# Kernel optimization log

Measured on AMD Instinct MI355X. Metric: run time of the kernel, lower is better.

Reference implementation:

```python
import jax, jax.numpy as jnp
import numpy as np

L = 3          # num_layers
H = 128        # hidden_dim
NH = 4         # num heads
DH = H // NH   # head dim
B = 32         # graphs per batch
N = 1024       # nodes per graph
NTOT = B * N
DEG = 16
E = NTOT * DEG
BN_EPS = 1e-5


def setup_inputs() -> dict:
    key = jax.random.key(0)
    ks = jax.random.split(key, 16)
    s = 1.0 / np.sqrt(H)
    inp = {
        "x": jax.random.normal(ks[0], (NTOT, H), jnp.float32),
        "edge_attr": jax.random.normal(ks[1], (E, H), jnp.float32),
        "gine_w1": jax.random.normal(ks[2], (L, H, H), jnp.float32) * s,
        "gine_b1": jnp.zeros((L, H), jnp.float32),
        "gine_bn_g": jnp.ones((L, H), jnp.float32),
        "gine_bn_b": jnp.zeros((L, H), jnp.float32),
        "gine_w2": jax.random.normal(ks[3], (L, H, H), jnp.float32) * s,
        "gine_b2": jnp.zeros((L, H), jnp.float32),
        "attn_wqkv": jax.random.normal(ks[4], (L, 3 * H, H), jnp.float32) * s,
        "attn_bqkv": jnp.zeros((L, 3 * H), jnp.float32),
        "attn_wo": jax.random.normal(ks[5], (L, H, H), jnp.float32) * s,
        "attn_bo": jnp.zeros((L, H), jnp.float32),
        "norm1_g": jnp.ones((L, H), jnp.float32),
        "norm1_b": jnp.zeros((L, H), jnp.float32),
        "norm2_g": jnp.ones((L, H), jnp.float32),
        "norm2_b": jnp.zeros((L, H), jnp.float32),
        "norm3_g": jnp.ones((L, H), jnp.float32),
        "norm3_b": jnp.zeros((L, H), jnp.float32),
        "mlp_w1": jax.random.normal(ks[6], (L, 2 * H, H), jnp.float32) * s,
        "mlp_b1": jnp.zeros((L, 2 * H), jnp.float32),
        "mlp_w2": jax.random.normal(ks[7], (L, H, 2 * H), jnp.float32) * (1.0 / np.sqrt(2 * H)),
        "mlp_b2": jnp.zeros((L, H), jnp.float32),
    }
    # intra-graph random edges: local src/dst in [0, N) plus per-graph offset
    offs = (jnp.arange(E, dtype=jnp.int32) // (N * DEG)) * N  # graph offset per edge
    src = jax.random.randint(ks[8], (E,), 0, N, jnp.int32) + offs
    dst = jax.random.randint(ks[9], (E,), 0, N, jnp.int32) + offs
    inp["edge_index"] = jnp.stack([src, dst]).astype(jnp.int32)
    inp["batch"] = (jnp.arange(NTOT, dtype=jnp.int32) // N)
    return inp


def _bn(x, g, b):
    m = x.mean(axis=0)
    v = jnp.var(x, axis=0)
    return (x - m) * jax.lax.rsqrt(v + BN_EPS) * g + b


def _gps_forward(x, edge_attr, gine_w1, gine_b1, gine_bn_g, gine_bn_b, gine_w2, gine_b2,
                 attn_wqkv, attn_bqkv, attn_wo, attn_bo,
                 norm1_g, norm1_b, norm2_g, norm2_b, norm3_g, norm3_b,
                 mlp_w1, mlp_b1, mlp_w2, mlp_b2, edge_index, batch):
    src, dst = edge_index[0], edge_index[1]
    for i in range(L):
        # ---- GINEConv: msg = relu(x_j + e), sum-scatter, nn-MLP on x + aggr (eps=0)
        msg = jax.nn.relu(x[src] + edge_attr)                       # [E, H]
        aggr = jax.ops.segment_sum(msg, dst, num_segments=NTOT)     # [NTOT, H]
        h = x + aggr
        h = h @ gine_w1[i].T + gine_b1[i]
        h = jax.nn.relu(_bn(h, gine_bn_g[i], gine_bn_b[i]))
        h = h @ gine_w2[i].T + gine_b2[i]
        h_local = _bn(h + x, norm1_g[i], norm1_b[i])                # residual + norm1
        # ---- global multi-head attention on x (dense per-graph, equal sizes)
        xb = x.reshape(B, N, H)
        qkv = xb @ attn_wqkv[i].T + attn_bqkv[i]                    # [B, N, 3H]
        q, k, v = jnp.split(qkv, 3, axis=-1)
        q = q.reshape(B, N, NH, DH).transpose(0, 2, 1, 3)           # [B, nh, N, dh]
        k = k.reshape(B, N, NH, DH).transpose(0, 2, 1, 3)
        v = v.reshape(B, N, NH, DH).transpose(0, 2, 1, 3)
        scores = jnp.einsum("bhqd,bhkd->bhqk", q, k) / np.sqrt(DH)
        attn = jax.nn.softmax(scores, axis=-1)
        o = jnp.einsum("bhqk,bhkd->bhqd", attn, v)
        o = o.transpose(0, 2, 1, 3).reshape(B, N, H) @ attn_wo[i].T + attn_bo[i]
        h_attn = _bn(o.reshape(NTOT, H) + x, norm2_g[i], norm2_b[i])
        # ---- combine + FFN + norm3
        out = h_local + h_attn
        ff = jax.nn.relu(out @ mlp_w1[i].T + mlp_b1[i]) @ mlp_w2[i].T + mlp_b2[i]
        x = _bn(out + ff, norm3_g[i], norm3_b[i])
        if i != L - 1:
            x = jax.nn.relu(x)
    return x


def reference(x, edge_attr, gine_w1, gine_b1, gine_bn_g, gine_bn_b, gine_w2, gine_b2,
              attn_wqkv, attn_bqkv, attn_wo, attn_bo,
              norm1_g, norm1_b, norm2_g, norm2_b, norm3_g, norm3_b,
              mlp_w1, mlp_b1, mlp_w2, mlp_b2, edge_index, batch):
    return _gps_forward(x, edge_attr, gine_w1, gine_b1, gine_bn_g, gine_bn_b, gine_w2, gine_b2,
                        attn_wqkv, attn_bqkv, attn_wo, attn_bo,
                        norm1_g, norm1_b, norm2_g, norm2_b, norm3_g, norm3_b,
                        mlp_w1, mlp_b1, mlp_w2, mlp_b2, edge_index, batch)
```

## Files before the change

kernel.cpp:

```cpp
#include <hip/hip_runtime.h>
#include <hip/hip_bf16.h>
#include <math.h>

#define NTOT 32768
#define HDIM 128
#define NE   524288
#define NGRAPH 32
#define NNODE 1024
#define NHEAD 4
#define DHEAD 32

typedef __attribute__((ext_vector_type(8))) short bf8v;
typedef __attribute__((ext_vector_type(4))) float f4v;
typedef unsigned short u16;

__device__ __forceinline__ float4 ld4(const float* p){ return *(const float4*)p; }

__device__ __forceinline__ u16 bf16rn(float f){
  union { float f; unsigned u; } x; x.f = f;
  unsigned r = x.u + 0x7FFF + ((x.u >> 16) & 1);
  return (u16)(r >> 16);
}
__device__ __forceinline__ unsigned pk2(float a, float b){
  unsigned r;
  asm("v_cvt_pk_bf16_f32 %0, %1, %2" : "=v"(r) : "v"(a), "v"(b));
  return r;
}
__device__ __forceinline__ float bf2f(u16 u){
  union { unsigned u; float f; } x; x.u = ((unsigned)u) << 16;
  return x.f;
}

__global__ void k_count(const int* __restrict__ dst, int* __restrict__ deg){
  int e = blockIdx.x*256 + threadIdx.x;
  atomicAdd(&deg[dst[e]], 1);
}

__global__ __launch_bounds__(1024) void k_scan(const int* __restrict__ deg,
                                               int* __restrict__ indptr,
                                               int* __restrict__ cursor){
  __shared__ int sm[1024];
  int t = threadIdx.x;
  int base = t*32;
  int s = 0;
  for (int j=0;j<32;j++) s += deg[base+j];
  sm[t] = s; __syncthreads();
  for (int off=1; off<1024; off<<=1){
    int v = (t>=off) ? sm[t-off] : 0;
    __syncthreads();
    sm[t] += v;
    __syncthreads();
  }
  int ex = sm[t] - s;
  for (int j=0;j<32;j++){
    int d = deg[base+j];
    indptr[base+j] = ex; cursor[base+j] = ex;
    ex += d;
  }
  if (t == 1023) indptr[NTOT] = ex;
}

__global__ void k_fill(const int* __restrict__ dst, int* __restrict__ cursor,
                       int* __restrict__ perm){
  int e = blockIdx.x*256 + threadIdx.x;
  int pos = atomicAdd(&cursor[dst[e]], 1);
  perm[pos] = e;
}

__global__ __launch_bounds__(256) void k_eaprep(const float* __restrict__ ea,
    const int* __restrict__ src, const int* __restrict__ perm,
    u16* __restrict__ EAb, int* __restrict__ SRCp){
  int tid = threadIdx.x;
  int p = blockIdx.x*8 + (tid>>5);
  int c4 = (tid&31)*4;
  int e = perm[p];
  float4 v = ld4(&ea[(size_t)e*HDIM + c4]);
  uint2 o; o.x = pk2(v.x, v.y); o.y = pk2(v.z, v.w);
  *(uint2*)&EAb[(size_t)p*HDIM + c4] = o;
  if ((tid&31) == 0) SRCp[p] = src[e];
}

__global__ __launch_bounds__(256) void k_xprep(const float* __restrict__ x, u16* __restrict__ Xb){
  size_t i = ((size_t)blockIdx.x*256 + threadIdx.x)*4;
  float4 v = ld4(&x[i]);
  uint2 o; o.x = pk2(v.x,v.y); o.y = pk2(v.z,v.w);
  *(uint2*)&Xb[i] = o;
}

__global__ __launch_bounds__(256) void k_wprep(const float* s0,const float* s1,const float* s2,
    const float* s3,const float* s4,const float* s5, u16* __restrict__ Wb){
  const float* srcs[6] = {s0,s1,s2,s3,s4,s5};
  const int cnt4[6] = {12288,12288,36864,12288,24576,24576};
  const int off[6]  = {0,49152,98304,245760,294912,393216};
  int y = blockIdx.y;
  int i = blockIdx.x*256 + threadIdx.x;
  if (i >= cnt4[y]) return;
  float4 v = ld4(&srcs[y][(size_t)i*4]);
  uint2 o; o.x = pk2(v.x,v.y); o.y = pk2(v.z,v.w);
  *(uint2*)&Wb[off[y] + (size_t)i*4] = o;
}

__global__ __launch_bounds__(256) void k_aggr(const u16* __restrict__ Xb,
                       const u16* __restrict__ EAb,
                       const int* __restrict__ SRCp, const int* __restrict__ indptr,
                       u16* __restrict__ Hb){
  int tid = threadIdx.x;
  int n = blockIdx.x*8 + (tid>>5);
  int c4 = (tid&31)*4;
  int p0 = indptr[n], p1 = indptr[n+1];
  float a0=0.f,a1=0.f,a2=0.f,a3=0.f;
  for (int p=p0;p<p1;p++){
    int s = SRCp[p];
    uint2 xv = *(const uint2*)&Xb[(size_t)s*HDIM + c4];
    uint2 ev = *(const uint2*)&EAb[(size_t)p*HDIM + c4];
    a0 += fmaxf(bf2f((u16)(xv.x&0xffff)) + bf2f((u16)(ev.x&0xffff)), 0.f);
    a1 += fmaxf(bf2f((u16)(xv.x>>16))    + bf2f((u16)(ev.x>>16)), 0.f);
    a2 += fmaxf(bf2f((u16)(xv.y&0xffff)) + bf2f((u16)(ev.y&0xffff)), 0.f);
    a3 += fmaxf(bf2f((u16)(xv.y>>16))    + bf2f((u16)(ev.y>>16)), 0.f);
  }
  uint2 xn = *(const uint2*)&Xb[(size_t)n*HDIM + c4];
  a0 += bf2f((u16)(xn.x&0xffff)); a1 += bf2f((u16)(xn.x>>16));
  a2 += bf2f((u16)(xn.y&0xffff)); a3 += bf2f((u16)(xn.y>>16));
  uint2 o; o.x = pk2(a0,a1); o.y = pk2(a2,a3);
  *(uint2*)&Hb[(size_t)n*HDIM + c4] = o;
}

template<bool BNA, bool DUAL, bool RELU, bool EP, bool STATS, bool WROUT>
__global__ __launch_bounds__(256) void k_bgemm(const u16* __restrict__ Ab,
    const u16* __restrict__ A2b,
    const float* __restrict__ slotA, const float* __restrict__ gA, const float* __restrict__ bA,
    const float* __restrict__ slotB, const float* __restrict__ gB, const float* __restrict__ bB,
    const u16* __restrict__ Wb, const float* __restrict__ bias,
    const u16* __restrict__ Epb, u16* __restrict__ Cb,
    u16* __restrict__ OUTb, float* __restrict__ slotOut, int N, int K){
  __shared__ float sbnA[256];
  __shared__ float sbnB[256];
  __shared__ float sred[128];
  int tid = threadIdx.x;
  int w = tid>>6, l = tid&63;
  int q = l&15, g = l>>4;
  int m0 = blockIdx.x*128, n0 = blockIdx.y*64;
  int wr = w*32;
  const float invn = 1.0f/32768.0f;
  if (BNA || DUAL){
    if (tid < 128){
      float mean = slotA[tid]*invn;
      float var  = slotA[128+tid]*invn - mean*mean;
      float sc = gA[tid] * rsqrtf(var + 1e-5f);
      sbnA[tid] = sc; sbnA[128+tid] = bA[tid] - mean*sc;
      if (DUAL){
        float mean2 = slotB[tid]*invn;
        float var2  = slotB[128+tid]*invn - mean2*mean2;
        float sc2 = gB[tid] * rsqrtf(var2 + 1e-5f);
        sbnB[tid] = sc2; sbnB[128+tid] = bB[tid] - mean2*sc2;
      }
    }
  }
  if (STATS && tid < 128) sred[tid] = 0.f;
  if (BNA || DUAL || STATS) __syncthreads();

  f4v acc[2][4];
  #pragma unroll
  for (int i=0;i<2;i++)
    #pragma unroll
    for (int j=0;j<4;j++) acc[i][j] = (f4v){0.f,0.f,0.f,0.f};

  for (int kc=0; kc<K; kc+=32){
    bf8v af[2], bfv[4];
    #pragma unroll
    for (int mt=0;mt<2;mt++){
      int row = m0 + wr + 16*mt + q;
      if (!BNA && !DUAL){
        af[mt] = *(const bf8v*)&Ab[(size_t)row*K + kc + 8*g];
      } else {
        union { bf8v b; u16 s[8]; unsigned u[4]; } ra, r2, ro;
        ra.b = *(const bf8v*)&Ab[(size_t)row*K + kc + 8*g];
        if (DUAL) r2.b = *(const bf8v*)&A2b[(size_t)row*K + kc + 8*g];
        float v[8];
        #pragma unroll
        for (int j=0;j<8;j++){
          int kk = kc + 8*g + j;
          float f = bf2f(ra.s[j]) * sbnA[kk] + sbnA[128+kk];
          if (BNA) f = fmaxf(f, 0.f);
          if (DUAL) f += bf2f(r2.s[j]) * sbnB[kk] + sbnB[128+kk];
          v[j] = f;
        }
        ro.u[0]=pk2(v[0],v[1]); ro.u[1]=pk2(v[2],v[3]);
        ro.u[2]=pk2(v[4],v[5]); ro.u[3]=pk2(v[6],v[7]);
        af[mt] = ro.b;
        if (WROUT && blockIdx.y == 0)
          *(uint4*)&OUTb[(size_t)row*K + kc + 8*g] = *(uint4*)ro.u;
      }
    }
    #pragma unroll
    for (int nt=0;nt<4;nt++){
      int col = n0 + 16*nt + q;
      bfv[nt] = *(const bf8v*)&Wb[(size_t)col*K + kc + 8*g];
    }
    #pragma unroll
    for (int mt=0;mt<2;mt++)
      #pragma unroll
      for (int nt=0;nt<4;nt++)
        acc[mt][nt] = __builtin_amdgcn_mfma_f32_16x16x32_bf16(af[mt], bfv[nt], acc[mt][nt], 0,0,0);
  }
  float bbv[4];
  #pragma unroll
  for (int nt=0;nt<4;nt++) bbv[nt] = bias[n0 + 16*nt + q];
  float csum[4] = {0.f,0.f,0.f,0.f}, csq[4] = {0.f,0.f,0.f,0.f};
  #pragma unroll
  for (int mt=0;mt<2;mt++){
    int row0 = m0 + wr + 16*mt + 4*g;
    #pragma unroll
    for (int nt=0;nt<4;nt++){
      int col = n0 + 16*nt + q;
      #pragma unroll
      for (int r=0;r<4;r++){
        size_t off = (size_t)(row0+r)*N + col;
        float v = acc[mt][nt][r] + bbv[nt];
        if (EP) v += bf2f(Epb[off]);
        if (RELU) v = fmaxf(v, 0.f);
        Cb[off] = bf16rn(v);
        if (STATS){ csum[nt] += v; csq[nt] += v*v; }
      }
    }
  }
  if (STATS){
    #pragma unroll
    for (int nt=0;nt<4;nt++){
      int c = 16*nt + q;
      atomicAdd(&sred[c], csum[nt]);
      atomicAdd(&sred[64+c], csq[nt]);
    }
    __syncthreads();
    if (tid < 64){
      atomicAdd(&slotOut[n0+tid], sred[tid]);
      atomicAdd(&slotOut[128+n0+tid], sred[64+tid]);
    }
  }
}

__global__ __launch_bounds__(256) void k_qkvgemm(const u16* __restrict__ Ab,
    const u16* __restrict__ Wb, const float* __restrict__ bias,
    u16* __restrict__ Qb, u16* __restrict__ Kb, u16* __restrict__ VT){
  __shared__ u16 Sm[128*72];
  int tid = threadIdx.x;
  int w = tid>>6, l = tid&63;
  int q = l&15, g = l>>4;
  int m0 = blockIdx.x*128, n0 = blockIdx.y*64;
  int which = blockIdx.y >> 1, half = blockIdx.y & 1;
  int wr = w*32;
  const int K = 128;
  f4v acc[2][4];
  #pragma unroll
  for (int i=0;i<2;i++)
    #pragma unroll
    for (int j=0;j<4;j++) acc[i][j] = (f4v){0.f,0.f,0.f,0.f};
  for (int kc=0; kc<K; kc+=32){
    bf8v af[2], bfv[4];
    #pragma unroll
    for (int mt=0;mt<2;mt++)
      af[mt] = *(const bf8v*)&Ab[(size_t)(m0+wr+16*mt+q)*K + kc + 8*g];
    #pragma unroll
    for (int nt=0;nt<4;nt++)
      bfv[nt] = *(const bf8v*)&Wb[(size_t)(n0+16*nt+q)*K + kc + 8*g];
    #pragma unroll
    for (int mt=0;mt<2;mt++)
      #pragma unroll
      for (int nt=0;nt<4;nt++)
        acc[mt][nt] = __builtin_amdgcn_mfma_f32_16x16x32_bf16(af[mt], bfv[nt], acc[mt][nt], 0,0,0);
  }
  const float QSC = 0.17677669529663687f * 1.4426950408889634f;
  float scale = (which==0) ? QSC : 1.0f;
  float bbv[4];
  #pragma unroll
  for (int nt=0;nt<4;nt++) bbv[nt] = bias[n0 + 16*nt + q];
  if (which < 2){
    #pragma unroll
    for (int mt=0;mt<2;mt++){
      int row0 = wr + 16*mt + 4*g;
      #pragma unroll
      for (int nt=0;nt<4;nt++){
        int c = 16*nt + q;
        #pragma unroll
        for (int r=0;r<4;r++)
          Sm[(row0+r)*72 + c] = bf16rn((acc[mt][nt][r] + bbv[nt]) * scale);
      }
    }
    __syncthreads();
    u16* dst = (which==0) ? Qb : Kb;
    #pragma unroll
    for (int it=0; it<4; it++){
      int idx = tid + it*256;
      int row = idx >> 3, c8 = (idx & 7) * 8;
      uint4 v = *(const uint4*)&Sm[row*72 + c8];
      *(uint4*)&dst[(size_t)(m0+row)*128 + half*64 + c8] = v;
    }
  } else {
    #pragma unroll
    for (int mt=0;mt<2;mt++){
      int row0 = wr + 16*mt + 4*g;
      #pragma unroll
      for (int nt=0;nt<4;nt++){
        int c = 16*nt + q;
        uint2 p;
        p.x = pk2(acc[mt][nt][0] + bbv[nt], acc[mt][nt][1] + bbv[nt]);
        p.y = pk2(acc[mt][nt][2] + bbv[nt], acc[mt][nt][3] + bbv[nt]);
        *(uint2*)&Sm[c*136 + row0] = p;
      }
    }
    __syncthreads();
    int gg = m0 >> 10;
    int nl0 = m0 - gg*1024;
    #pragma unroll
    for (int it=0; it<4; it++){
      int idx = tid + it*256;
      int c = idx >> 4, n8 = (idx & 15) * 8;
      uint4 v = *(const uint4*)&Sm[c*136 + n8];
      *(uint4*)&VT[((size_t)gg*128 + half*64 + c)*1024 + nl0 + n8] = v;
    }
  }
}

template<bool RELU, bool F32OUT>
__global__ __launch_bounds__(256) void k_bnapply(const u16* __restrict__ X,
    const float* __restrict__ slot, const float* __restrict__ gv, const float* __restrict__ bv,
    u16* __restrict__ Yb, float* __restrict__ Yf){
  int idx = blockIdx.x*256 + threadIdx.x;
  int row = idx >> 4, c8 = (idx & 15) * 8;
  const float invn = 1.0f/32768.0f;
  union { uint4 u; u16 s[8]; } iv;
  iv.u = *(const uint4*)&X[(size_t)row*HDIM + c8];
  float o[8];
  #pragma unroll
  for (int j=0;j<8;j++){
    int c = c8+j;
    float mean = slot[c]*invn;
    float var  = slot[128+c]*invn - mean*mean;
    float sc = gv[c] * rsqrtf(var + 1e-5f);
    float sh = bv[c] - mean*sc;
    float v = bf2f(iv.s[j])*sc + sh;
    if (RELU) v = fmaxf(v, 0.f);
    o[j] = v;
  }
  if (F32OUT){
    float* dst = &Yf[(size_t)row*HDIM + c8];
    *(float4*)dst = make_float4(o[0],o[1],o[2],o[3]);
    *(float4*)(dst+4) = make_float4(o[4],o[5],o[6],o[7]);
  } else {
    uint4 ov;
    ov.x = pk2(o[0],o[1]); ov.y = pk2(o[2],o[3]);
    ov.z = pk2(o[4],o[5]); ov.w = pk2(o[6],o[7]);
    *(uint4*)&Yb[(size_t)row*HDIM + c8] = ov;
  }
}

__global__ __launch_bounds__(256) void k_flash2(const u16* __restrict__ Qb,
    const u16* __restrict__ Kb, const u16* __restrict__ VT,
    u16* __restrict__ O){
  __shared__ u16 Pl[4][16*72];
  int tid = threadIdx.x;
  int w = tid >> 6, l = tid & 63;
  int q = l & 15, grp = l >> 4;
  int qt = blockIdx.x, h = blockIdx.y, g = blockIdx.z;
  size_t gbase = (size_t)g*1024;
  size_t qrow0 = gbase + qt*64 + w*16;
  const u16* Vp = VT + ((size_t)(g*4 + h)*32)*1024;
  bf8v qf = *(const bf8v*)&Qb[(qrow0 + q)*128 + h*32 + 8*grp];
  u16* Pw = &Pl[w][0];
  float m = -1e30f, lsum = 0.f;
  f4v o0 = {0.f,0.f,0.f,0.f}, o1 = {0.f,0.f,0.f,0.f};
  for (int kt=0; kt<16; kt++){
    int k0 = kt*64;
    f4v st[4];
    #pragma unroll
    for (int t=0;t<4;t++){
      bf8v kf = *(const bf8v*)&Kb[(gbase + k0 + 16*t + q)*128 + h*32 + 8*grp];
      st[t] = __builtin_amdgcn_mfma_f32_16x16x32_bf16(kf, qf, (f4v){0.f,0.f,0.f,0.f}, 0,0,0);
    }
    float smax = st[0][0];
    #pragma unroll
    for (int t=0;t<4;t++)
      #pragma unroll
      for (int r=0;r<4;r++) smax = fmaxf(smax, st[t][r]);
    smax = fmaxf(smax, __shfl_xor(smax, 16));
    smax = fmaxf(smax, __shfl_xor(smax, 32));
    float mnew = fmaxf(m, smax);
    float alpha = exp2f(m - mnew);
    float psum = 0.f;
    #pragma unroll
    for (int t=0;t<4;t++){
      float p0 = exp2f(st[t][0]-mnew), p1 = exp2f(st[t][1]-mnew);
      float p2 = exp2f(st[t][2]-mnew), p3 = exp2f(st[t][3]-mnew);
      psum += (p0+p1)+(p2+p3);
      *(unsigned*)&Pw[q*72 + 16*t + 4*grp]     = pk2(p0,p1);
      *(unsigned*)&Pw[q*72 + 16*t + 4*grp + 2] = pk2(p2,p3);
    }
    psum += __shfl_xor(psum, 16);
    psum += __shfl_xor(psum, 32);
    lsum = lsum*alpha + psum;
    m = mnew;
    f4v aD;
    #pragma unroll
    for (int r=0;r<4;r++) aD[r] = __shfl(alpha, 4*grp + r);
    #pragma unroll
    for (int r=0;r<4;r++){ o0[r] *= aD[r]; o1[r] *= aD[r]; }
    bf8v pa0 = *(const bf8v*)&Pw[q*72 + 8*grp];
    bf8v pa1 = *(const bf8v*)&Pw[q*72 + 32 + 8*grp];
    bf8v v00 = *(const bf8v*)&Vp[(size_t)q*1024      + k0 + 8*grp];
    bf8v v01 = *(const bf8v*)&Vp[(size_t)q*1024      + k0 + 32 + 8*grp];
    bf8v v10 = *(const bf8v*)&Vp[(size_t)(16+q)*1024 + k0 + 8*grp];
    bf8v v11 = *(const bf8v*)&Vp[(size_t)(16+q)*1024 + k0 + 32 + 8*grp];
    o0 = __builtin_amdgcn_mfma_f32_16x16x32_bf16(pa0, v00, o0, 0,0,0);
    o0 = __builtin_amdgcn_mfma_f32_16x16x32_bf16(pa1, v01, o0, 0,0,0);
    o1 = __builtin_amdgcn_mfma_f32_16x16x32_bf16(pa0, v10, o1, 0,0,0);
    o1 = __builtin_amdgcn_mfma_f32_16x16x32_bf16(pa1, v11, o1, 0,0,0);
  }
  f4v lD;
  #pragma unroll
  for (int r=0;r<4;r++) lD[r] = __shfl(lsum, 4*grp + r);
  #pragma unroll
  for (int r=0;r<4;r++){
    float inv = 1.0f/lD[r];
    size_t row = qrow0 + 4*grp + r;
    O[row*HDIM + h*32 + q]      = bf16rn(o0[r]*inv);
    O[row*HDIM + h*32 + 16 + q] = bf16rn(o1[r]*inv);
  }
}

extern "C" void kernel_launch(void* const* d_in, const int* in_sizes, int n_in,
                              void* d_out, int out_size, void* d_ws, size_t ws_size,
                              hipStream_t stream){
  const float* x_in      = (const float*)d_in[0];
  const float* edge_attr = (const float*)d_in[1];
  const float* gine_w1   = (const float*)d_in[2];
  const float* gine_b1   = (const float*)d_in[3];
  const float* gine_bn_g = (const float*)d_in[4];
  const float* gine_bn_b = (const float*)d_in[5];
  const float* gine_w2   = (const float*)d_in[6];
  const float* gine_b2   = (const float*)d_in[7];
  const float* attn_wqkv = (const float*)d_in[8];
  const float* attn_bqkv = (const float*)d_in[9];
  const float* attn_wo   = (const float*)d_in[10];
  const float* attn_bo   = (const float*)d_in[11];
  const float* norm1_g   = (const float*)d_in[12];
  const float* norm1_b   = (const float*)d_in[13];
  const float* norm2_g   = (const float*)d_in[14];
  const float* norm2_b   = (const float*)d_in[15];
  const float* norm3_g   = (const float*)d_in[16];
  const float* norm3_b   = (const float*)d_in[17];
  const float* mlp_w1    = (const float*)d_in[18];
  const float* mlp_b1    = (const float*)d_in[19];
  const float* mlp_w2    = (const float*)d_in[20];
  const float* mlp_b2    = (const float*)d_in[21];
  const int* edge_index  = (const int*)d_in[22];
  const int* srcp = edge_index;
  const int* dstp = edge_index + NE;
  float* out = (float*)d_out;

  float* ws = (float*)d_ws;
  const size_t U = 4194304;
  u16* Xb   = (u16*)(ws);
  u16* Hb   = (u16*)(ws + U/2);
  u16* G1   = (u16*)(ws + U);
  u16* P1   = (u16*)(ws + U + U/2);
  u16* P2   = (u16*)(ws + 2*U);
  u16* Ob   = (u16*)(ws + 2*U + U/2);
  u16* FFb  = (u16*)(ws + 3*U);
  u16* OUTb = (u16*)(ws + 4*U);
  u16* H3   = (u16*)(ws + 4*U + U/2);
  u16* Qb   = (u16*)(ws + 5*U);
  u16* Kb   = (u16*)(ws + 5*U + U/2);
  u16* VTb  = (u16*)(ws + 6*U);
  u16* Wball= (u16*)(ws + 6*U + U/2);
  float* STATS = ws + 7*U - 8192;
  int* IW      = (int*)(ws + 7*U);
  int* deg     = IW;
  int* indptr  = IW + 32768;
  int* cursor  = IW + 32768 + 32772;
  int* perm    = cursor + 32768;
  u16* EAb  = (u16*)(ws + 8*U);
  int* SRCp = (int*)(ws + 16*U);

  u16* W1b  = Wball + 0;
  u16* W2b  = Wball + 49152;
  u16* WQb  = Wball + 98304;
  u16* WOb  = Wball + 245760;
  u16* WM1b = Wball + 294912;
  u16* WM2b = Wball + 393216;

  hipMemsetAsync(STATS, 0, 12*512*sizeof(float), stream);
  hipMemsetAsync(deg, 0, NTOT*sizeof(int), stream);
  k_count<<<NE/256, 256, 0, stream>>>(dstp, deg);
  k_scan<<<1, 1024, 0, stream>>>(deg, indptr, cursor);
  k_fill<<<NE/256, 256, 0, stream>>>(dstp, cursor, perm);
  k_eaprep<<<NE/8, 256, 0, stream>>>(edge_attr, srcp, perm, EAb, SRCp);
  k_xprep<<<4096, 256, 0, stream>>>(x_in, Xb);
  k_wprep<<<dim3(144,6), 256, 0, stream>>>(gine_w1, gine_w2, attn_wqkv, attn_wo, mlp_w1, mlp_w2, Wball);

  dim3 gN128(NTOT/128, 2), gN256(NTOT/128, 4), gQKV(NTOT/128, 6);

  for (int i=0;i<3;i++){
    const float* B1 = gine_b1 + (size_t)i*HDIM;
    const float* B2 = gine_b2 + (size_t)i*HDIM;
    const float* BQ = attn_bqkv + (size_t)i*3*HDIM;
    const float* BO = attn_bo + (size_t)i*HDIM;
    const float* BM1 = mlp_b1 + (size_t)i*2*HDIM;
    const float* BM2 = mlp_b2 + (size_t)i*HDIM;
    u16* w1 = W1b + (size_t)i*16384;
    u16* w2 = W2b + (size_t)i*16384;
    u16* wq = WQb + (size_t)i*49152;
    u16* wo = WOb + (size_t)i*16384;
    u16* wm1 = WM1b + (size_t)i*32768;
    u16* wm2 = WM2b + (size_t)i*32768;
    float* S0 = STATS + (size_t)(i*4+0)*512;
    float* S1 = STATS + (size_t)(i*4+1)*512;
    float* S2 = STATS + (size_t)(i*4+2)*512;
    float* S3 = STATS + (size_t)(i*4+3)*512;
    const float* bnG = gine_bn_g + (size_t)i*HDIM;
    const float* bnB = gine_bn_b + (size_t)i*HDIM;
    const float* n1g = norm1_g + (size_t)i*HDIM, *n1b = norm1_b + (size_t)i*HDIM;
    const float* n2g = norm2_g + (size_t)i*HDIM, *n2b = norm2_b + (size_t)i*HDIM;
    const float* n3g = norm3_g + (size_t)i*HDIM, *n3b = norm3_b + (size_t)i*HDIM;

    k_aggr<<<NTOT/8, 256, 0, stream>>>(Xb, EAb, SRCp, indptr, Hb);
    k_bgemm<false,false,false,false,true,false><<<gN128, 256, 0, stream>>>(
      Hb, nullptr, nullptr,nullptr,nullptr, nullptr,nullptr,nullptr,
      w1, B1, nullptr, G1, nullptr, S0, 128, 128);
    k_bgemm<true,false,false,true,true,false><<<gN128, 256, 0, stream>>>(
      G1, nullptr, S0, bnG, bnB, nullptr,nullptr,nullptr,
      w2, B2, Xb, P1, nullptr, S1, 128, 128);

    k_qkvgemm<<<gQKV, 256, 0, stream>>>(Xb, wq, BQ, Qb, Kb, VTb);
    k_flash2<<<dim3(16, NHEAD, NGRAPH), 256, 0, stream>>>(Qb, Kb, VTb, Ob);
    k_bgemm<false,false,false,true,true,false><<<gN128, 256, 0, stream>>>(
      Ob, nullptr, nullptr,nullptr,nullptr, nullptr,nullptr,nullptr,
      wo, BO, Xb, P2, nullptr, S2, 128, 128);

    k_bgemm<false,true,true,false,false,true><<<gN256, 256, 0, stream>>>(
      P1, P2, S1, n1g, n1b, S2, n2g, n2b,
      wm1, BM1, nullptr, FFb, OUTb, nullptr, 256, 128);
    k_bgemm<false,false,false,true,true,false><<<gN128, 256, 0, stream>>>(
      FFb, nullptr, nullptr,nullptr,nullptr, nullptr,nullptr,nullptr,
      wm2, BM2, OUTb, H3, nullptr, S3, 128, 256);

    if (i<2) k_bnapply<true ,false><<<2048, 256, 0, stream>>>(H3, S3, n3g, n3b, Xb, nullptr);
    else     k_bnapply<false,true ><<<2048, 256, 0, stream>>>(H3, S3, n3g, n3b, nullptr, out);
  }
}
```

Before: 1.049 ms.

## Retile GEMMs to 32x128 blocks, split aggregation per wave, merge prep kernels

The batched GEMM and QKV GEMM tiles change from 128x64 to 32x128 per block. Each wave now covers 16 rows by 64 columns, so every block spans the full 128-column output, and the stats reduction and QKV staging are adjusted to match. The aggregation kernel gives each node one wave whose two halves handle alternating edges, prefetches the next source index, and combines the halves with a shuffle. The three prep kernels become one launch and the two memsets become one, cutting launch overhead at the cost of more blocks and less A-operand reuse per block.

After: 1.310 ms. 1.25x slower.

```diff
diff --git a/kernel.cpp b/kernel.cpp
--- a/kernel.cpp
+++ b/kernel.cpp
@@ -67,62 +67,71 @@
   perm[pos] = e;
 }
 
-__global__ __launch_bounds__(256) void k_eaprep(const float* __restrict__ ea,
+__global__ __launch_bounds__(256) void k_prep(const float* __restrict__ ea,
     const int* __restrict__ src, const int* __restrict__ perm,
-    u16* __restrict__ EAb, int* __restrict__ SRCp){
+    u16* __restrict__ EAb, int* __restrict__ SRCp,
+    const float* __restrict__ x, u16* __restrict__ Xb,
+    const float* s0,const float* s1,const float* s2,
+    const float* s3,const float* s4,const float* s5, u16* __restrict__ Wb){
+  int b = blockIdx.x, tid = threadIdx.x;
+  if (b < 65536){
+    int p = b*8 + (tid>>5);
+    int c4 = (tid&31)*4;
+    int e = perm[p];
+    float4 v = ld4(&ea[(size_t)e*HDIM + c4]);
+    uint2 o; o.x = pk2(v.x, v.y); o.y = pk2(v.z, v.w);
+    *(uint2*)&EAb[(size_t)p*HDIM + c4] = o;
+    if ((tid&31) == 0) SRCp[p] = src[e];
+  } else if (b < 69632){
+    size_t i = ((size_t)(b-65536)*256 + tid)*4;
+    float4 v = ld4(&x[i]);
+    uint2 o; o.x = pk2(v.x,v.y); o.y = pk2(v.z,v.w);
+    *(uint2*)&Xb[i] = o;
+  } else {
+    int idx = b - 69632;
+    int y = idx / 144;
+    int i = (idx % 144)*256 + tid;
+    const float* srcs[6] = {s0,s1,s2,s3,s4,s5};
+    const int cnt4[6] = {12288,12288,36864,12288,24576,24576};
+    const int off[6]  = {0,49152,98304,245760,294912,393216};
+    if (i < cnt4[y]){
+      float4 v = ld4(&srcs[y][(size_t)i*4]);
+      uint2 o; o.x = pk2(v.x,v.y); o.y = pk2(v.z,v.w);
+      *(uint2*)&Wb[off[y] + (size_t)i*4] = o;
+    }
+  }
+}
+
+__global__ __launch_bounds__(256) void k_aggr(const u16* __restrict__ Xb,
+    const u16* __restrict__ EAb, const int* __restrict__ SRCp,
+    const int* __restrict__ indptr, u16* __restrict__ Hb){
   int tid = threadIdx.x;
-  int p = blockIdx.x*8 + (tid>>5);
-  int c4 = (tid&31)*4;
-  int e = perm[p];
-  float4 v = ld4(&ea[(size_t)e*HDIM + c4]);
-  uint2 o; o.x = pk2(v.x, v.y); o.y = pk2(v.z, v.w);
-  *(uint2*)&EAb[(size_t)p*HDIM + c4] = o;
-  if ((tid&31) == 0) SRCp[p] = src[e];
-}
-
-__global__ __launch_bounds__(256) void k_xprep(const float* __restrict__ x, u16* __restrict__ Xb){
-  size_t i = ((size_t)blockIdx.x*256 + threadIdx.x)*4;
-  float4 v = ld4(&x[i]);
-  uint2 o; o.x = pk2(v.x,v.y); o.y = pk2(v.z,v.w);
-  *(uint2*)&Xb[i] = o;
-}
-
-__global__ __launch_bounds__(256) void k_wprep(const float* s0,const float* s1,const float* s2,
-    const float* s3,const float* s4,const float* s5, u16* __restrict__ Wb){
-  const float* srcs[6] = {s0,s1,s2,s3,s4,s5};
-  const int cnt4[6] = {12288,12288,36864,12288,24576,24576};
-  const int off[6]  = {0,49152,98304,245760,294912,393216};
-  int y = blockIdx.y;
-  int i = blockIdx.x*256 + threadIdx.x;
-  if (i >= cnt4[y]) return;
-  float4 v = ld4(&srcs[y][(size_t)i*4]);
-  uint2 o; o.x = pk2(v.x,v.y); o.y = pk2(v.z,v.w);
-  *(uint2*)&Wb[off[y] + (size_t)i*4] = o;
-}
-
-__global__ __launch_bounds__(256) void k_aggr(const u16* __restrict__ Xb,
-                       const u16* __restrict__ EAb,
-                       const int* __restrict__ SRCp, const int* __restrict__ indptr,
-                       u16* __restrict__ Hb){
-  int tid = threadIdx.x;
-  int n = blockIdx.x*8 + (tid>>5);
-  int c4 = (tid&31)*4;
+  int w = tid>>6, lane = tid&63, half = lane>>5, cl = lane&31;
+  int c4 = cl*4;
+  int n = blockIdx.x*4 + w;
   int p0 = indptr[n], p1 = indptr[n+1];
   float a0=0.f,a1=0.f,a2=0.f,a3=0.f;
-  for (int p=p0;p<p1;p++){
-    int s = SRCp[p];
+  int p = p0 + half;
+  int sNext = (p < p1) ? SRCp[p] : 0;
+  for (; p < p1; p += 2){
+    int s = sNext;
+    if (p+2 < p1) sNext = SRCp[p+2];
+    uint2 ev = *(const uint2*)&EAb[(size_t)p*HDIM + c4];
     uint2 xv = *(const uint2*)&Xb[(size_t)s*HDIM + c4];
-    uint2 ev = *(const uint2*)&EAb[(size_t)p*HDIM + c4];
     a0 += fmaxf(bf2f((u16)(xv.x&0xffff)) + bf2f((u16)(ev.x&0xffff)), 0.f);
     a1 += fmaxf(bf2f((u16)(xv.x>>16))    + bf2f((u16)(ev.x>>16)), 0.f);
     a2 += fmaxf(bf2f((u16)(xv.y&0xffff)) + bf2f((u16)(ev.y&0xffff)), 0.f);
     a3 += fmaxf(bf2f((u16)(xv.y>>16))    + bf2f((u16)(ev.y>>16)), 0.f);
   }
-  uint2 xn = *(const uint2*)&Xb[(size_t)n*HDIM + c4];
-  a0 += bf2f((u16)(xn.x&0xffff)); a1 += bf2f((u16)(xn.x>>16));
-  a2 += bf2f((u16)(xn.y&0xffff)); a3 += bf2f((u16)(xn.y>>16));
-  uint2 o; o.x = pk2(a0,a1); o.y = pk2(a2,a3);
-  *(uint2*)&Hb[(size_t)n*HDIM + c4] = o;
+  a0 += __shfl_xor(a0, 32); a1 += __shfl_xor(a1, 32);
+  a2 += __shfl_xor(a2, 32); a3 += __shfl_xor(a3, 32);
+  if (half == 0){
+    uint2 xn = *(const uint2*)&Xb[(size_t)n*HDIM + c4];
+    a0 += bf2f((u16)(xn.x&0xffff)); a1 += bf2f((u16)(xn.x>>16));
+    a2 += bf2f((u16)(xn.y&0xffff)); a3 += bf2f((u16)(xn.y>>16));
+    uint2 o; o.x = pk2(a0,a1); o.y = pk2(a2,a3);
+    *(uint2*)&Hb[(size_t)n*HDIM + c4] = o;
+  }
 }
 
 template<bool BNA, bool DUAL, bool RELU, bool EP, bool STATS, bool WROUT>
@@ -133,108 +142,93 @@
     const u16* __restrict__ Wb, const float* __restrict__ bias,
     const u16* __restrict__ Epb, u16* __restrict__ Cb,
     u16* __restrict__ OUTb, float* __restrict__ slotOut, int N, int K){
-  __shared__ float sbnA[256];
-  __shared__ float sbnB[256];
-  __shared__ float sred[128];
+  __shared__ float sbn1[256];
+  __shared__ float sbn2[256];
+  __shared__ float sred[256];
   int tid = threadIdx.x;
   int w = tid>>6, l = tid&63;
   int q = l&15, g = l>>4;
-  int m0 = blockIdx.x*128, n0 = blockIdx.y*64;
-  int wr = w*32;
+  int rh = w&1, ch = w>>1;
+  int m0 = blockIdx.x*32, n0 = blockIdx.y*128;
   const float invn = 1.0f/32768.0f;
-  if (BNA || DUAL){
+  if ((BNA || DUAL) && tid < 128){
+    float mean = slotA[tid]*invn;
+    float var  = slotA[128+tid]*invn - mean*mean;
+    float s = gA[tid] * rsqrtf(var + 1e-5f);
+    sbn1[tid] = s; sbn1[128+tid] = bA[tid] - mean*s;
+    if (DUAL){
+      float mean2 = slotB[tid]*invn;
+      float var2  = slotB[128+tid]*invn - mean2*mean2;
+      float s2 = gB[tid] * rsqrtf(var2 + 1e-5f);
+      sbn2[tid] = s2; sbn2[128+tid] = bB[tid] - mean2*s2;
+    }
+  }
+  if (STATS && tid < 128){ sred[tid] = 0.f; sred[128+tid] = 0.f; }
+  if (BNA || DUAL || STATS) __syncthreads();
+
+  f4v acc[4];
+  #pragma unroll
+  for (int j=0;j<4;j++) acc[j] = (f4v){0.f,0.f,0.f,0.f};
+
+  int row = m0 + rh*16 + q;
+  for (int kc=0; kc<K; kc+=32){
+    bf8v af;
+    if (!BNA && !DUAL){
+      af = *(const bf8v*)&Ab[(size_t)row*K + kc + 8*g];
+    } else {
+      union { bf8v b; u16 s[8]; unsigned u[4]; } ra, r2, ro;
+      ra.b = *(const bf8v*)&Ab[(size_t)row*K + kc + 8*g];
+      if (DUAL) r2.b = *(const bf8v*)&A2b[(size_t)row*K + kc + 8*g];
+      float v[8];
+      #pragma unroll
+      for (int j=0;j<8;j++){
+        int kk = kc + 8*g + j;
+        float f = bf2f(ra.s[j]) * sbn1[kk] + sbn1[128+kk];
+        if (BNA) f = fmaxf(f, 0.f);
+        if (DUAL) f += bf2f(r2.s[j]) * sbn2[kk] + sbn2[128+kk];
+        v[j] = f;
+      }
+      ro.u[0]=pk2(v[0],v[1]); ro.u[1]=pk2(v[2],v[3]);
+      ro.u[2]=pk2(v[4],v[5]); ro.u[3]=pk2(v[6],v[7]);
+      af = ro.b;
+      if (WROUT && blockIdx.y == 0 && ch == 0)
+        *(uint4*)&OUTb[(size_t)row*K + kc + 8*g] = *(uint4*)ro.u;
+    }
+    #pragma unroll
+    for (int nt=0;nt<4;nt++){
+      bf8v bv = *(const bf8v*)&Wb[(size_t)(n0 + ch*64 + 16*nt + q)*K + kc + 8*g];
+      acc[nt] = __builtin_amdgcn_mfma_f32_16x16x32_bf16(af, bv, acc[nt], 0,0,0);
+    }
+  }
+  float bbv[4];
+  #pragma unroll
+  for (int nt=0;nt<4;nt++) bbv[nt] = bias[n0 + ch*64 + 16*nt + q];
+  int row0 = m0 + rh*16 + 4*g;
+  float csum[4] = {0.f,0.f,0.f,0.f}, csq[4] = {0.f,0.f,0.f,0.f};
+  #pragma unroll
+  for (int nt=0;nt<4;nt++){
+    int col = n0 + ch*64 + 16*nt + q;
+    #pragma unroll
+    for (int r=0;r<4;r++){
+      size_t off = (size_t)(row0+r)*N + col;
+      float v = acc[nt][r] + bbv[nt];
+      if (EP) v += bf2f(Epb[off]);
+      if (RELU) v = fmaxf(v, 0.f);
+      Cb[off] = bf16rn(v);
+      if (STATS){ csum[nt] += v; csq[nt] += v*v; }
+    }
+  }
+  if (STATS){
+    #pragma unroll
+    for (int nt=0;nt<4;nt++){
+      int c = (ch*64 + 16*nt + q) & 127;
+      atomicAdd(&sred[c], csum[nt]);
+      atomicAdd(&sred[128+c], csq[nt]);
+    }
+    __syncthreads();
     if (tid < 128){
-      float mean = slotA[tid]*invn;
-      float var  = slotA[128+tid]*invn - mean*mean;
-      float sc = gA[tid] * rsqrtf(var + 1e-5f);
-      sbnA[tid] = sc; sbnA[128+tid] = bA[tid] - mean*sc;
-      if (DUAL){
-        float mean2 = slotB[tid]*invn;
-        float var2  = slotB[128+tid]*invn - mean2*mean2;
-        float sc2 = gB[tid] * rsqrtf(var2 + 1e-5f);
-        sbnB[tid] = sc2; sbnB[128+tid] = bB[tid] - mean2*sc2;
-      }
-    }
-  }
-  if (STATS && tid < 128) sred[tid] = 0.f;
-  if (BNA || DUAL || STATS) __syncthreads();
-
-  f4v acc[2][4];
-  #pragma unroll
-  for (int i=0;i<2;i++)
-    #pragma unroll
-    for (int j=0;j<4;j++) acc[i][j] = (f4v){0.f,0.f,0.f,0.f};
-
-  for (int kc=0; kc<K; kc+=32){
-    bf8v af[2], bfv[4];
-    #pragma unroll
-    for (int mt=0;mt<2;mt++){
-      int row = m0 + wr + 16*mt + q;
-      if (!BNA && !DUAL){
-        af[mt] = *(const bf8v*)&Ab[(size_t)row*K + kc + 8*g];
-      } else {
-        union { bf8v b; u16 s[8]; unsigned u[4]; } ra, r2, ro;
-        ra.b = *(const bf8v*)&Ab[(size_t)row*K + kc + 8*g];
-        if (DUAL) r2.b = *(const bf8v*)&A2b[(size_t)row*K + kc + 8*g];
-        float v[8];
-        #pragma unroll
-        for (int j=0;j<8;j++){
-          int kk = kc + 8*g + j;
-          float f = bf2f(ra.s[j]) * sbnA[kk] + sbnA[128+kk];
-          if (BNA) f = fmaxf(f, 0.f);
-          if (DUAL) f += bf2f(r2.s[j]) * sbnB[kk] + sbnB[128+kk];
-          v[j] = f;
-        }
-        ro.u[0]=pk2(v[0],v[1]); ro.u[1]=pk2(v[2],v[3]);
-        ro.u[2]=pk2(v[4],v[5]); ro.u[3]=pk2(v[6],v[7]);
-        af[mt] = ro.b;
-        if (WROUT && blockIdx.y == 0)
-          *(uint4*)&OUTb[(size_t)row*K + kc + 8*g] = *(uint4*)ro.u;
-      }
-    }
-    #pragma unroll
-    for (int nt=0;nt<4;nt++){
-      int col = n0 + 16*nt + q;
-      bfv[nt] = *(const bf8v*)&Wb[(size_t)col*K + kc + 8*g];
-    }
-    #pragma unroll
-    for (int mt=0;mt<2;mt++)
-      #pragma unroll
-      for (int nt=0;nt<4;nt++)
-        acc[mt][nt] = __builtin_amdgcn_mfma_f32_16x16x32_bf16(af[mt], bfv[nt], acc[mt][nt], 0,0,0);
-  }
-  float bbv[4];
-  #pragma unroll
-  for (int nt=0;nt<4;nt++) bbv[nt] = bias[n0 + 16*nt + q];
-  float csum[4] = {0.f,0.f,0.f,0.f}, csq[4] = {0.f,0.f,0.f,0.f};
-  #pragma unroll
-  for (int mt=0;mt<2;mt++){
-    int row0 = m0 + wr + 16*mt + 4*g;
-    #pragma unroll
-    for (int nt=0;nt<4;nt++){
-      int col = n0 + 16*nt + q;
-      #pragma unroll
-      for (int r=0;r<4;r++){
-        size_t off = (size_t)(row0+r)*N + col;
-        float v = acc[mt][nt][r] + bbv[nt];
-        if (EP) v += bf2f(Epb[off]);
-        if (RELU) v = fmaxf(v, 0.f);
-        Cb[off] = bf16rn(v);
-        if (STATS){ csum[nt] += v; csq[nt] += v*v; }
-      }
-    }
-  }
-  if (STATS){
-    #pragma unroll
-    for (int nt=0;nt<4;nt++){
-      int c = 16*nt + q;
-      atomicAdd(&sred[c], csum[nt]);
-      atomicAdd(&sred[64+c], csq[nt]);
-    }
-    __syncthreads();
-    if (tid < 64){
-      atomicAdd(&slotOut[n0+tid], sred[tid]);
-      atomicAdd(&slotOut[128+n0+tid], sred[64+tid]);
+      atomicAdd(&slotOut[tid], sred[tid]);
+      atomicAdd(&slotOut[128+tid], sred[128+tid]);
     }
   }
 }
@@ -242,81 +236,67 @@
 __global__ __launch_bounds__(256) void k_qkvgemm(const u16* __restrict__ Ab,
     const u16* __restrict__ Wb, const float* __restrict__ bias,
     u16* __restrict__ Qb, u16* __restrict__ Kb, u16* __restrict__ VT){
-  __shared__ u16 Sm[128*72];
+  __shared__ u16 Sm[5120];
   int tid = threadIdx.x;
   int w = tid>>6, l = tid&63;
   int q = l&15, g = l>>4;
-  int m0 = blockIdx.x*128, n0 = blockIdx.y*64;
-  int which = blockIdx.y >> 1, half = blockIdx.y & 1;
-  int wr = w*32;
+  int rh = w&1, ch = w>>1;
+  int which = blockIdx.y;
+  int m0 = blockIdx.x*32, n0 = which*128;
   const int K = 128;
-  f4v acc[2][4];
-  #pragma unroll
-  for (int i=0;i<2;i++)
-    #pragma unroll
-    for (int j=0;j<4;j++) acc[i][j] = (f4v){0.f,0.f,0.f,0.f};
+  f4v acc[4];
+  #pragma unroll
+  for (int j=0;j<4;j++) acc[j] = (f4v){0.f,0.f,0.f,0.f};
+  int row = m0 + rh*16 + q;
   for (int kc=0; kc<K; kc+=32){
-    bf8v af[2], bfv[4];
-    #pragma unroll
-    for (int mt=0;mt<2;mt++)
-      af[mt] = *(const bf8v*)&Ab[(size_t)(m0+wr+16*mt+q)*K + kc + 8*g];
-    #pragma unroll
-    for (int nt=0;nt<4;nt++)
-      bfv[nt] = *(const bf8v*)&Wb[(size_t)(n0+16*nt+q)*K + kc + 8*g];
-    #pragma unroll
-    for (int mt=0;mt<2;mt++)
-      #pragma unroll
-      for (int nt=0;nt<4;nt++)
-        acc[mt][nt] = __builtin_amdgcn_mfma_f32_16x16x32_bf16(af[mt], bfv[nt], acc[mt][nt], 0,0,0);
+    bf8v af = *(const bf8v*)&Ab[(size_t)row*K + kc + 8*g];
+    #pragma unroll
+    for (int nt=0;nt<4;nt++){
+      bf8v bv = *(const bf8v*)&Wb[(size_t)(n0 + ch*64 + 16*nt + q)*K + kc + 8*g];
+      acc[nt] = __builtin_amdgcn_mfma_f32_16x16x32_bf16(af, bv, acc[nt], 0,0,0);
+    }
   }
   const float QSC = 0.17677669529663687f * 1.4426950408889634f;
   float scale = (which==0) ? QSC : 1.0f;
   float bbv[4];
   #pragma unroll
-  for (int nt=0;nt<4;nt++) bbv[nt] = bias[n0 + 16*nt + q];
+  for (int nt=0;nt<4;nt++) bbv[nt] = bias[n0 + ch*64 + 16*nt + q];
+  int row0l = rh*16 + 4*g;
   if (which < 2){
     #pragma unroll
-    for (int mt=0;mt<2;mt++){
-      int row0 = wr + 16*mt + 4*g;
+    for (int nt=0;nt<4;nt++){
+      int c = ch*64 + 16*nt + q;
       #pragma unroll
-      for (int nt=0;nt<4;nt++){
-        int c = 16*nt + q;
-        #pragma unroll
-        for (int r=0;r<4;r++)
-          Sm[(row0+r)*72 + c] = bf16rn((acc[mt][nt][r] + bbv[nt]) * scale);
-      }
+      for (int r=0;r<4;r++)
+        Sm[(row0l+r)*136 + c] = bf16rn((acc[nt][r] + bbv[nt]) * scale);
     }
     __syncthreads();
     u16* dst = (which==0) ? Qb : Kb;
     #pragma unroll
-    for (int it=0; it<4; it++){
+    for (int it=0; it<2; it++){
       int idx = tid + it*256;
-      int row = idx >> 3, c8 = (idx & 7) * 8;
-      uint4 v = *(const uint4*)&Sm[row*72 + c8];
-      *(uint4*)&dst[(size_t)(m0+row)*128 + half*64 + c8] = v;
+      int rr = idx >> 4, c8 = (idx & 15) * 8;
+      uint4 v = *(const uint4*)&Sm[rr*136 + c8];
+      *(uint4*)&dst[(size_t)(m0+rr)*128 + c8] = v;
     }
   } else {
     #pragma unroll
-    for (int mt=0;mt<2;mt++){
-      int row0 = wr + 16*mt + 4*g;
-      #pragma unroll
-      for (int nt=0;nt<4;nt++){
-        int c = 16*nt + q;
-        uint2 p;
-        p.x = pk2(acc[mt][nt][0] + bbv[nt], acc[mt][nt][1] + bbv[nt]);
-        p.y = pk2(acc[mt][nt][2] + bbv[nt], acc[mt][nt][3] + bbv[nt]);
-        *(uint2*)&Sm[c*136 + row0] = p;
-      }
+    for (int nt=0;nt<4;nt++){
+      int c = ch*64 + 16*nt + q;
+      uint2 p;
+      p.x = pk2(acc[nt][0] + bbv[nt], acc[nt][1] + bbv[nt]);
+      p.y = pk2(acc[nt][2] + bbv[nt], acc[nt][3] + bbv[nt]);
+      *(uint2*)&Sm[c*40 + row0l] = p;
     }
     __syncthreads();
     int gg = m0 >> 10;
-    int nl0 = m0 - gg*1024;
-    #pragma unroll
-    for (int it=0; it<4; it++){
+    int nl0 = m0 & 1023;
+    #pragma unroll
+    for (int it=0; it<2; it++){
       int idx = tid + it*256;
-      int c = idx >> 4, n8 = (idx & 15) * 8;
-      uint4 v = *(const uint4*)&Sm[c*136 + n8];
-      *(uint4*)&VT[((size_t)gg*128 + half*64 + c)*1024 + nl0 + n8] = v;
+      int c = idx >> 2, n8 = (idx & 3) * 8;
+      uint4 v = *(const uint4*)&Sm[c*40 + n8];
+      *(uint4*)&VT[((size_t)gg*128 + c)*1024 + nl0 + n8] = v;
     }
   }
 }
@@ -488,16 +468,16 @@
   u16* WM1b = Wball + 294912;
   u16* WM2b = Wball + 393216;
 
-  hipMemsetAsync(STATS, 0, 12*512*sizeof(float), stream);
-  hipMemsetAsync(deg, 0, NTOT*sizeof(int), stream);
+  hipMemsetAsync(STATS, 0, 8192*sizeof(float) + NTOT*sizeof(int), stream);
   k_count<<<NE/256, 256, 0, stream>>>(dstp, deg);
   k_scan<<<1, 1024, 0, stream>>>(deg, indptr, cursor);
   k_fill<<<NE/256, 256, 0, stream>>>(dstp, cursor, perm);
-  k_eaprep<<<NE/8, 256, 0, stream>>>(edge_attr, srcp, perm, EAb, SRCp);
-  k_xprep<<<4096, 256, 0, stream>>>(x_in, Xb);
-  k_wprep<<<dim3(144,6), 256, 0, stream>>>(gine_w1, gine_w2, attn_wqkv, attn_wo, mlp_w1, mlp_w2, Wball);
-
-  dim3 gN128(NTOT/128, 2), gN256(NTOT/128, 4), gQKV(NTOT/128, 6);
+  k_prep<<<70496, 256, 0, stream>>>(edge_attr, srcp, perm, EAb, SRCp, x_in, Xb,
+                                    gine_w1, gine_w2, attn_wqkv, attn_wo, mlp_w1, mlp_w2, Wball);
+
+  const u16* NUL16 = nullptr;
+  const float* NULF = nullptr;
+  dim3 g1(NTOT/32, 1), g2(NTOT/32, 2), gq(NTOT/32, 3);
 
   for (int i=0;i<3;i++){
     const float* B1 = gine_b1 + (size_t)i*HDIM;
@@ -522,25 +502,25 @@
     const float* n2g = norm2_g + (size_t)i*HDIM, *n2b = norm2_b + (size_t)i*HDIM;
     const float* n3g = norm3_g + (size_t)i*HDIM, *n3b = norm3_b + (size_t)i*HDIM;
 
-    k_aggr<<<NTOT/8, 256, 0, stream>>>(Xb, EAb, SRCp, indptr, Hb);
-    k_bgemm<false,false,false,false,true,false><<<gN128, 256, 0, stream>>>(
-      Hb, nullptr, nullptr,nullptr,nullptr, nullptr,nullptr,nullptr,
-      w1, B1, nullptr, G1, nullptr, S0, 128, 128);
-    k_bgemm<true,false,false,true,true,false><<<gN128, 256, 0, stream>>>(
-      G1, nullptr, S0, bnG, bnB, nullptr,nullptr,nullptr,
+    k_aggr<<<NTOT/4, 256, 0, stream>>>(Xb, EAb, SRCp, indptr, Hb);
+    k_bgemm<false,false,false,false,true,false><<<g1, 256, 0, stream>>>(
+      Hb, NUL16, NULF,NULF,NULF, NULF,NULF,NULF,
+      w1, B1, NUL16, G1, nullptr, S0, 128, 128);
+    k_bgemm<true,false,false,true,true,false><<<g1, 256, 0, stream>>>(
+      G1, NUL16, S0, bnG, bnB, NULF,NULF,NULF,
       w2, B2, Xb, P1, nullptr, S1, 128, 128);
 
-    k_qkvgemm<<<gQKV, 256, 0, stream>>>(Xb, wq, BQ, Qb, Kb, VTb);
+    k_qkvgemm<<<gq, 256, 0, stream>>>(Xb, wq, BQ, Qb, Kb, VTb);
     k_flash2<<<dim3(16, NHEAD, NGRAPH), 256, 0, stream>>>(Qb, Kb, VTb, Ob);
-    k_bgemm<false,false,false,true,true,false><<<gN128, 256, 0, stream>>>(
-      Ob, nullptr, nullptr,nullptr,nullptr, nullptr,nullptr,nullptr,
+    k_bgemm<false,false,false,true,true,false><<<g1, 256, 0, stream>>>(
+      Ob, NUL16, NULF,NULF,NULF, NULF,NULF,NULF,
       wo, BO, Xb, P2, nullptr, S2, 128, 128);
 
-    k_bgemm<false,true,true,false,false,true><<<gN256, 256, 0, stream>>>(
+    k_bgemm<false,true,true,false,false,true><<<g2, 256, 0, stream>>>(
       P1, P2, S1, n1g, n1b, S2, n2g, n2b,
-      wm1, BM1, nullptr, FFb, OUTb, nullptr, 256, 128);
-    k_bgemm<false,false,false,true,true,false><<<gN128, 256, 0, stream>>>(
-      FFb, nullptr, nullptr,nullptr,nullptr, nullptr,nullptr,nullptr,
+      wm1, BM1, NUL16, FFb, OUTb, nullptr, 256, 128);
+    k_bgemm<false,false,false,true,true,false><<<g1, 256, 0, stream>>>(
+      FFb, NUL16, NULF,NULF,NULF, NULF,NULF,NULF,
       wm2, BM2, OUTb, H3, nullptr, S3, 128, 256);
 
     if (i<2) k_bnapply<true ,false><<<2048, 256, 0, stream>>>(H3, S3, n3g, n3b, Xb, nullptr);
```
